# Kernel optimization log

Hardware: AMD Instinct MI355X
Metric: run time of the kernel (lower is better)

The kernel has to match this reference:

```python
import jax, jax.numpy as jnp
import numpy as np

E = 8        # number of sessions (experts)
N = 512      # per-session input width (max units)
P = 512      # n_channels (output width)
F = 100      # max_F time bins
B = 128      # batch of trials
SCALE = 1.0


def setup_inputs() -> dict:
    key = jax.random.key(0)
    kx, ke, k1, k2, k3, k4 = jax.random.split(key, 6)
    x = jax.random.normal(kx, (B, F, N), dtype=jnp.float32)
    eid = jax.random.randint(ke, (B,), 0, E, dtype=jnp.int32)
    # Per-session stitcher Linear(N, 2N) and projector Linear(2N, P), stacked.
    s1 = 1.0 / np.sqrt(N)
    s2 = 1.0 / np.sqrt(2 * N)
    W1 = jax.random.uniform(k1, (E, N, 2 * N), jnp.float32, -s1, s1)
    b1 = jax.random.uniform(k2, (E, 2 * N), jnp.float32, -s1, s1)
    W2 = jax.random.uniform(k3, (E, 2 * N, P), jnp.float32, -s2, s2)
    b2 = jax.random.uniform(k4, (E, P), jnp.float32, -s2, s2)
    return {"x": x, "eid": eid, "W1": W1, "b1": b1, "W2": W2, "b2": b2}


def reference(x, eid, W1, b1, W2, b2):
    # Grouped (per-session) Linear -> Softsign -> Linear, dispatched by eid.
    # Equivalent to the torch loop over unique eids with mask gather/scatter,
    # expressed as a gather of per-sample expert weights + batched matmul.
    w1 = W1[eid]                      # [B, N, 2N]
    stitched = jnp.einsum('bfn,bnh->bfh', x, w1) + b1[eid][:, None, :]
    act = stitched / (1.0 + jnp.abs(stitched))  # Softsign
    act = act * SCALE
    w2 = W2[eid]                      # [B, 2N, P]
    out = jnp.einsum('bfh,bhp->bfp', act, w2) + b2[eid][:, None, :]
    return out                        # [B, F, P]
```

## Files before the change

### kernel.cpp

```cpp
#include <hip/hip_runtime.h>
#include <hip/hip_bf16.h>

#define B_ 128
#define F_ 100
#define N_ 512
#define H_ 1024
#define P_ 512
#define E_ 8

#define BM 128
#define BK 64

typedef __attribute__((ext_vector_type(8))) short bf16x8;
typedef __attribute__((ext_vector_type(4))) float f32x4;

#define GLOAD16(g, l) __builtin_amdgcn_global_load_lds(                      \
    (const __attribute__((address_space(1))) void*)(g),                      \
    (__attribute__((address_space(3))) void*)(l), 16, 0, 0)

static __device__ __forceinline__ short f2bf(float f) {
    __hip_bfloat16 h = __float2bfloat16(f);
    short s;
    __builtin_memcpy(&s, &h, sizeof(s));
    return s;
}

__global__ __launch_bounds__(128) void sort_eid(const int* __restrict__ eid,
                                                int* __restrict__ perm,
                                                int* __restrict__ esort) {
    __shared__ int cnt[E_], base[E_];
    const int t = threadIdx.x;
    if (t < E_) cnt[t] = 0;
    __syncthreads();
    const int e = eid[t];
    atomicAdd(&cnt[e], 1);
    __syncthreads();
    if (t == 0) {
        int s = 0;
        for (int i = 0; i < E_; i++) { base[i] = s; s += cnt[i]; }
    }
    __syncthreads();
    const int pos = atomicAdd(&base[e], 1);
    perm[pos] = t;
    esort[pos] = e;
}

__global__ __launch_bounds__(256) void convert_x(const float* __restrict__ x,
                                                 const int* __restrict__ perm,
                                                 short* __restrict__ xs) {
    const int g = blockIdx.x * 256 + threadIdx.x;
    const int col = (g & (N_ / 8 - 1)) * 8;
    const int row = g >> 6;
    const int f = row & 127, sp = row >> 7;
    union { short s[8]; uint4 u; } o;
    if (f < F_) {
        const int b = perm[sp];
        const float* xp = x + ((size_t)(b * F_ + f)) * N_ + col;
        const float4 v0 = *(const float4*)(xp);
        const float4 v1 = *(const float4*)(xp + 4);
        o.s[0] = f2bf(v0.x); o.s[1] = f2bf(v0.y);
        o.s[2] = f2bf(v0.z); o.s[3] = f2bf(v0.w);
        o.s[4] = f2bf(v1.x); o.s[5] = f2bf(v1.y);
        o.s[6] = f2bf(v1.z); o.s[7] = f2bf(v1.w);
    } else {
        o.u = make_uint4(0u, 0u, 0u, 0u);
    }
    *(uint4*)(xs + (size_t)row * N_ + col) = o.u;
}

__global__ __launch_bounds__(256) void transpose_cvt(const float* __restrict__ W,
                                                     short* __restrict__ WT,
                                                     int R, int C) {
    __shared__ float tile[64][65];
    const int e = blockIdx.z;
    const int c0 = blockIdx.x * 64, r0 = blockIdx.y * 64;
    const int t = threadIdx.x;
    const float* Wp = W + (size_t)e * R * C;
    short* WTp = WT + (size_t)e * C * R;
    {
        const int c4 = (t & 15) * 4, r = t >> 4;
#pragma unroll
        for (int p = 0; p < 4; p++) {
            const int row = p * 16 + r;
            const float4 v = *(const float4*)(Wp + (size_t)(r0 + row) * C + c0 + c4);
            tile[row][c4 + 0] = v.x; tile[row][c4 + 1] = v.y;
            tile[row][c4 + 2] = v.z; tile[row][c4 + 3] = v.w;
        }
    }
    __syncthreads();
    {
        const int r8 = (t & 7) * 8, cl = t >> 3;
#pragma unroll
        for (int p = 0; p < 2; p++) {
            const int c = p * 32 + cl;
            union { short s[8]; uint4 u; } o;
#pragma unroll
            for (int j = 0; j < 8; j++) o.s[j] = f2bf(tile[r8 + j][c]);
            *(uint4*)(&WTp[(size_t)(c0 + c) * R + r0 + r8]) = o.u;
        }
    }
}

template <int KDIM, int BN_, bool FIRST>
__global__ __launch_bounds__(256, 4) void gemm_kernel(
    const short* __restrict__ A,
    const short* __restrict__ WT,
    const float* __restrict__ bias,
    const int* __restrict__ perm,
    const int* __restrict__ esort,
    short* __restrict__ actout,
    float* __restrict__ out)
{
    constexpr int NCOLS = FIRST ? H_ : P_;
    constexpr int NI = BN_ / 32;
    __shared__ short sA[BM * BK];
    __shared__ short sB[BN_ * BK];
    const int sp = (blockIdx.x & 7) * 16 + (blockIdx.x >> 3);
    const int n0 = blockIdx.y * BN_;
    const int e = esort[sp];
    const int t = threadIdx.x;
    const int lane = t & 63, w = t >> 6;
    const int wm = (w >> 1) * 64, wn = (w & 1) * (BN_ / 2);
    const int l15 = lane & 15, quad = lane >> 4;
    const int lr = lane >> 3;
    const int lc = (((lane & 7) ^ lr) * 8);

    f32x4 acc[4][NI];
#pragma unroll
    for (int mi = 0; mi < 4; mi++)
#pragma unroll
        for (int ni = 0; ni < NI; ni++)
            acc[mi][ni] = (f32x4)(0.0f);

    const short* Ap = A + (size_t)sp * BM * KDIM;
    const short* Bp = WT + ((size_t)e * NCOLS + n0) * KDIM;

    for (int k0 = 0; k0 < KDIM; k0 += BK) {
#pragma unroll
        for (int i = 0; i < 4; i++) {
            const int rb = w * 32 + i * 8;
            GLOAD16(Ap + (size_t)(rb + lr) * KDIM + k0 + lc, &sA[rb * BK]);
        }
#pragma unroll
        for (int i = 0; i < BN_ / 32; i++) {
            const int rb = w * (BN_ / 4) + i * 8;
            GLOAD16(Bp + (size_t)(rb + lr) * KDIM + k0 + lc, &sB[rb * BK]);
        }
        __syncthreads();
#pragma unroll
        for (int ks = 0; ks < 2; ks++) {
            bf16x8 af[4], bfr[NI];
#pragma unroll
            for (int mi = 0; mi < 4; mi++) {
                const int ra = wm + mi * 16 + l15;
                af[mi] = *(const bf16x8*)(&sA[ra * BK + (((ks * 4 + quad) ^ (ra & 7)) * 8)]);
            }
#pragma unroll
            for (int ni = 0; ni < NI; ni++) {
                const int rbn = wn + ni * 16 + l15;
                bfr[ni] = *(const bf16x8*)(&sB[rbn * BK + (((ks * 4 + quad) ^ (rbn & 7)) * 8)]);
            }
#pragma unroll
            for (int mi = 0; mi < 4; mi++)
#pragma unroll
                for (int ni = 0; ni < NI; ni++)
                    acc[mi][ni] = __builtin_amdgcn_mfma_f32_16x16x32_bf16(af[mi], bfr[ni], acc[mi][ni], 0, 0, 0);
        }
        __syncthreads();
    }

    const int borig = FIRST ? 0 : perm[sp];
#pragma unroll
    for (int mi = 0; mi < 4; mi++) {
#pragma unroll
        for (int ni = 0; ni < NI; ni++) {
            const int col = n0 + wn + ni * 16 + l15;
            const float bv = bias[(size_t)e * NCOLS + col];
#pragma unroll
            for (int r = 0; r < 4; r++) {
                const int row = wm + mi * 16 + quad * 4 + r;
                float v = acc[mi][ni][r] + bv;
                if constexpr (FIRST) {
                    v = v / (1.0f + fabsf(v));
                    actout[((size_t)sp * BM + row) * H_ + col] = f2bf(v);
                } else {
                    if (row < F_)
                        out[((size_t)borig * F_ + row) * P_ + col] = v;
                }
            }
        }
    }
}

extern "C" void kernel_launch(void* const* d_in, const int* in_sizes, int n_in,
                              void* d_out, int out_size, void* d_ws, size_t ws_size,
                              hipStream_t stream) {
    const float* x  = (const float*)d_in[0];
    const int* eid  = (const int*)d_in[1];
    const float* W1 = (const float*)d_in[2];
    const float* b1 = (const float*)d_in[3];
    const float* W2 = (const float*)d_in[4];
    const float* b2 = (const float*)d_in[5];
    float* out = (float*)d_out;

    char* ws = (char*)d_ws;
    short* W1T = (short*)(ws);
    short* W2T = (short*)(ws + (size_t)(8u << 20));
    short* act = (short*)(ws + (size_t)(16u << 20));
    short* xs  = (short*)(ws + (size_t)(48u << 20));
    int* perm  = (int*)(ws + (size_t)(64u << 20));
    int* esort = perm + B_;

    sort_eid<<<1, 128, 0, stream>>>(eid, perm, esort);
    convert_x<<<dim3((B_ * 128 * N_ / 8) / 256), 256, 0, stream>>>(x, perm, xs);
    transpose_cvt<<<dim3(H_ / 64, N_ / 64, E_), 256, 0, stream>>>(W1, W1T, N_, H_);
    transpose_cvt<<<dim3(P_ / 64, H_ / 64, E_), 256, 0, stream>>>(W2, W2T, H_, P_);
    gemm_kernel<N_, 128, true><<<dim3(B_, H_ / 128), 256, 0, stream>>>(xs, W1T, b1, perm, esort, act, nullptr);
    gemm_kernel<H_, 64, false><<<dim3(B_, P_ / 64), 256, 0, stream>>>(act, W2T, b2, perm, esort, nullptr, out);
}
```

Before: 158.3 us.

## Pack rows densely per expert and merge weight prep with sort

Replaces per-sample 128-row tiles (each padded from 100 rows) with dense per-expert row packing. A tile table lists M-tiles over the concatenated rows of each expert group. This removes the padded MFMA work and the padded activation traffic. The sort and both weight transposes are fused into one prep kernel, which cuts launches, and convert_x now writes only real rows. The cost is extra division and modulo in the epilogues and some idle blocks that exit early.

```diff
diff --git a/kernel.cpp b/kernel.cpp
--- a/kernel.cpp
+++ b/kernel.cpp
@@ -10,6 +10,9 @@
 
 #define BM 128
 #define BK 64
+#define ROWS (B_ * F_)
+#define RPAD (ROWS + 128)
+#define MT_MAX 112
 
 typedef __attribute__((ext_vector_type(8))) short bf16x8;
 typedef __attribute__((ext_vector_type(4))) float f32x4;
@@ -25,55 +28,23 @@
     return s;
 }
 
-__global__ __launch_bounds__(128) void sort_eid(const int* __restrict__ eid,
-                                                int* __restrict__ perm,
-                                                int* __restrict__ esort) {
-    __shared__ int cnt[E_], base[E_];
-    const int t = threadIdx.x;
-    if (t < E_) cnt[t] = 0;
-    __syncthreads();
-    const int e = eid[t];
-    atomicAdd(&cnt[e], 1);
-    __syncthreads();
-    if (t == 0) {
-        int s = 0;
-        for (int i = 0; i < E_; i++) { base[i] = s; s += cnt[i]; }
-    }
-    __syncthreads();
-    const int pos = atomicAdd(&base[e], 1);
-    perm[pos] = t;
-    esort[pos] = e;
-}
-
-__global__ __launch_bounds__(256) void convert_x(const float* __restrict__ x,
-                                                 const int* __restrict__ perm,
-                                                 short* __restrict__ xs) {
-    const int g = blockIdx.x * 256 + threadIdx.x;
-    const int col = (g & (N_ / 8 - 1)) * 8;
-    const int row = g >> 6;
-    const int f = row & 127, sp = row >> 7;
-    union { short s[8]; uint4 u; } o;
-    if (f < F_) {
-        const int b = perm[sp];
-        const float* xp = x + ((size_t)(b * F_ + f)) * N_ + col;
-        const float4 v0 = *(const float4*)(xp);
-        const float4 v1 = *(const float4*)(xp + 4);
-        o.s[0] = f2bf(v0.x); o.s[1] = f2bf(v0.y);
-        o.s[2] = f2bf(v0.z); o.s[3] = f2bf(v0.w);
-        o.s[4] = f2bf(v1.x); o.s[5] = f2bf(v1.y);
-        o.s[6] = f2bf(v1.z); o.s[7] = f2bf(v1.w);
+__global__ __launch_bounds__(256) void prep_weights(
+    const float* __restrict__ W1, const float* __restrict__ W2,
+    short* __restrict__ W1T, short* __restrict__ W2T,
+    const int* __restrict__ eid, int* __restrict__ perm,
+    int4* __restrict__ ttab) {
+    __shared__ float tile[64][65];
+    __shared__ int scnt[E_], sbase[E_];
+    const int e = blockIdx.z;
+    const float* W; short* WT; int R, C, c0, r0;
+    if (blockIdx.y < 8) {
+        W = W1; WT = W1T; R = N_; C = H_;
+        c0 = blockIdx.x * 64; r0 = blockIdx.y * 64;
     } else {
-        o.u = make_uint4(0u, 0u, 0u, 0u);
-    }
-    *(uint4*)(xs + (size_t)row * N_ + col) = o.u;
-}
-
-__global__ __launch_bounds__(256) void transpose_cvt(const float* __restrict__ W,
-                                                     short* __restrict__ WT,
-                                                     int R, int C) {
-    __shared__ float tile[64][65];
-    const int e = blockIdx.z;
-    const int c0 = blockIdx.x * 64, r0 = blockIdx.y * 64;
+        W = W2; WT = W2T; R = H_; C = P_;
+        c0 = (blockIdx.x & 7) * 64;
+        r0 = ((blockIdx.y - 8) * 2 + (blockIdx.x >> 3)) * 64;
+    }
     const int t = threadIdx.x;
     const float* Wp = W + (size_t)e * R * C;
     short* WTp = WT + (size_t)e * C * R;
@@ -99,6 +70,54 @@
             *(uint4*)(&WTp[(size_t)(c0 + c) * R + r0 + r8]) = o.u;
         }
     }
+    if (blockIdx.x == 0 && blockIdx.y == 0 && blockIdx.z == 0) {
+        __syncthreads();
+        if (t < E_) scnt[t] = 0;
+        __syncthreads();
+        int my_e = 0;
+        if (t < B_) { my_e = eid[t]; atomicAdd(&scnt[my_e], 1); }
+        __syncthreads();
+        if (t == 0) {
+            int s = 0;
+            for (int i = 0; i < E_; i++) { sbase[i] = s; s += scnt[i]; }
+        }
+        __syncthreads();
+        if (t < B_) {
+            const int pos = atomicAdd(&sbase[my_e], 1);
+            perm[pos] = t;
+        }
+        if (t == 0) {
+            int tix = 0, s = 0;
+            for (int e2 = 0; e2 < E_; e2++) {
+                const int c = scnt[e2];
+                const int r1 = (s + c) * F_;
+                for (int m0 = s * F_; m0 < r1; m0 += BM)
+                    ttab[tix++] = make_int4(m0, min(m0 + BM, r1), e2, 0);
+                s += c;
+            }
+            for (; tix < MT_MAX; tix++) ttab[tix] = make_int4(1 << 30, 0, 0, 0);
+        }
+    }
+}
+
+__global__ __launch_bounds__(256) void convert_x(const float* __restrict__ x,
+                                                 const int* __restrict__ perm,
+                                                 short* __restrict__ xs) {
+    const int gs = (blockIdx.x & 7) * 400 + (blockIdx.x >> 3);
+    const int g = gs * 256 + threadIdx.x;
+    const int col = (g & (N_ / 8 - 1)) * 8;
+    const int row = g >> 6;
+    const int sp = row / F_, f = row % F_;
+    const int b = perm[sp];
+    const float* xp = x + ((size_t)(b * F_ + f)) * N_ + col;
+    const float4 v0 = *(const float4*)(xp);
+    const float4 v1 = *(const float4*)(xp + 4);
+    union { short s[8]; uint4 u; } o;
+    o.s[0] = f2bf(v0.x); o.s[1] = f2bf(v0.y);
+    o.s[2] = f2bf(v0.z); o.s[3] = f2bf(v0.w);
+    o.s[4] = f2bf(v1.x); o.s[5] = f2bf(v1.y);
+    o.s[6] = f2bf(v1.z); o.s[7] = f2bf(v1.w);
+    *(uint4*)(xs + (size_t)row * N_ + col) = o.u;
 }
 
 template <int KDIM, int BN_, bool FIRST>
@@ -107,7 +126,7 @@
     const short* __restrict__ WT,
     const float* __restrict__ bias,
     const int* __restrict__ perm,
-    const int* __restrict__ esort,
+    const int4* __restrict__ ttab,
     short* __restrict__ actout,
     float* __restrict__ out)
 {
@@ -115,9 +134,11 @@
     constexpr int NI = BN_ / 32;
     __shared__ short sA[BM * BK];
     __shared__ short sB[BN_ * BK];
-    const int sp = (blockIdx.x & 7) * 16 + (blockIdx.x >> 3);
+    const int xt = (blockIdx.x & 7) * 14 + (blockIdx.x >> 3);
+    const int4 tt = ttab[xt];
+    if (tt.x >= ROWS) return;
+    const int m0 = tt.x, me = tt.y, e = tt.z;
     const int n0 = blockIdx.y * BN_;
-    const int e = esort[sp];
     const int t = threadIdx.x;
     const int lane = t & 63, w = t >> 6;
     const int wm = (w >> 1) * 64, wn = (w & 1) * (BN_ / 2);
@@ -132,7 +153,7 @@
         for (int ni = 0; ni < NI; ni++)
             acc[mi][ni] = (f32x4)(0.0f);
 
-    const short* Ap = A + (size_t)sp * BM * KDIM;
+    const short* Ap = A + (size_t)m0 * KDIM;
     const short* Bp = WT + ((size_t)e * NCOLS + n0) * KDIM;
 
     for (int k0 = 0; k0 < KDIM; k0 += BK) {
@@ -169,7 +190,6 @@
         __syncthreads();
     }
 
-    const int borig = FIRST ? 0 : perm[sp];
 #pragma unroll
     for (int mi = 0; mi < 4; mi++) {
 #pragma unroll
@@ -178,14 +198,16 @@
             const float bv = bias[(size_t)e * NCOLS + col];
 #pragma unroll
             for (int r = 0; r < 4; r++) {
-                const int row = wm + mi * 16 + quad * 4 + r;
-                float v = acc[mi][ni][r] + bv;
-                if constexpr (FIRST) {
-                    v = v / (1.0f + fabsf(v));
-                    actout[((size_t)sp * BM + row) * H_ + col] = f2bf(v);
-                } else {
-                    if (row < F_)
-                        out[((size_t)borig * F_ + row) * P_ + col] = v;
+                const int grow = m0 + wm + mi * 16 + quad * 4 + r;
+                if (grow < me) {
+                    float v = acc[mi][ni][r] + bv;
+                    if constexpr (FIRST) {
+                        v = v / (1.0f + fabsf(v));
+                        actout[(size_t)grow * H_ + col] = f2bf(v);
+                    } else {
+                        const int sp = grow / F_, f = grow % F_;
+                        out[((size_t)perm[sp] * F_ + f) * P_ + col] = v;
+                    }
                 }
             }
         }
@@ -207,14 +229,12 @@
     short* W1T = (short*)(ws);
     short* W2T = (short*)(ws + (size_t)(8u << 20));
     short* act = (short*)(ws + (size_t)(16u << 20));
-    short* xs  = (short*)(ws + (size_t)(48u << 20));
-    int* perm  = (int*)(ws + (size_t)(64u << 20));
-    int* esort = perm + B_;
-
-    sort_eid<<<1, 128, 0, stream>>>(eid, perm, esort);
-    convert_x<<<dim3((B_ * 128 * N_ / 8) / 256), 256, 0, stream>>>(x, perm, xs);
-    transpose_cvt<<<dim3(H_ / 64, N_ / 64, E_), 256, 0, stream>>>(W1, W1T, N_, H_);
-    transpose_cvt<<<dim3(P_ / 64, H_ / 64, E_), 256, 0, stream>>>(W2, W2T, H_, P_);
-    gemm_kernel<N_, 128, true><<<dim3(B_, H_ / 128), 256, 0, stream>>>(xs, W1T, b1, perm, esort, act, nullptr);
-    gemm_kernel<H_, 64, false><<<dim3(B_, P_ / 64), 256, 0, stream>>>(act, W2T, b2, perm, esort, nullptr, out);
-}
+    short* xs  = (short*)(ws + (size_t)(44u << 20));
+    int*  perm = (int*)(ws + (size_t)(58u << 20));
+    int4* ttab = (int4*)(ws + (size_t)(58u << 20) + 1024);
+
+    prep_weights<<<dim3(16, 16, E_), 256, 0, stream>>>(W1, W2, W1T, W2T, eid, perm, ttab);
+    convert_x<<<dim3(ROWS * N_ / 8 / 256), 256, 0, stream>>>(x, perm, xs);
+    gemm_kernel<N_, 128, true><<<dim3(MT_MAX, H_ / 128), 256, 0, stream>>>(xs, W1T, b1, perm, ttab, act, nullptr);
+    gemm_kernel<H_, 64, false><<<dim3(MT_MAX, P_ / 64), 256, 0, stream>>>(act, W2T, b2, perm, ttab, nullptr, out);
+}
```

Measured after the change: 162.0 us. +2.3%, slower.
